# Kernel optimization log

Measured on AMD Instinct MI355X. Metric: run time of the kernel, lower is better.

Reference implementation:

```python
import jax, jax.numpy as jnp
import numpy as np

KERNEL = 3
PAD = (KERNEL - 1) // 2  # non-causal symmetric padding


def setup_inputs() -> dict:
    key = jax.random.key(0)
    k1, k2, k3 = jax.random.split(key, 3)
    B, Cin, Cout, S = 16, 64, 64, 1024
    return {
        "input": jax.random.normal(k1, (B, Cin, S), dtype=jnp.float32),
        "weight": jax.random.normal(k2, (Cout, Cin, S, KERNEL), dtype=jnp.float32),
        "bias": jax.random.normal(k3, (Cout, S), dtype=jnp.float32),
    }


def reference(input, weight, bias):
    # input: (B, Cin, S); weight: (Cout, Cin, S, K); bias: (Cout, S)
    S = input.shape[-1]
    padded = jnp.pad(input, ((0, 0), (0, 0), (PAD, PAD)))
    # unfolded windows: (B, Cin, S, K) -- small, avoids the (B,Cout,Cin,S,K) blowup
    unfolded = jnp.stack([padded[:, :, k:k + S] for k in range(KERNEL)], axis=-1)
    # position-specific (non-weight-shared) conv: contract Cin and K per position s
    out = jnp.einsum("bcsk,ocsk->bos", unfolded, weight)
    return out + bias[None, :, :]
```

## Files before the change

kernel.cpp:

```cpp
#include <hip/hip_runtime.h>

namespace {
constexpr int CIN = 64, COUT = 64, SS = 1024, KK = 3;
constexpr int STL = 16;
constexpr int CCH = 8;
constexpr int POS = STL + 2;
constexpr int RST = 20;
}

__global__ __launch_bounds__(256, 2)
void locon1d(const float* __restrict__ in, const float* __restrict__ wt,
             const float* __restrict__ bias, float* __restrict__ out) {
  __shared__ float xs[CCH * POS * RST];

  const int tid = threadIdx.x;
  const int sl  = tid & 15;
  const int og  = tid >> 4;
  const int bid = blockIdx.x;
  const int st  = bid & 63;
  const int ch  = bid >> 6;
  const int s0  = st * STL;
  const int s   = s0 + sl;
  const int cb  = ch * CCH;
  const int o0  = og * 4;

  #pragma unroll
  for (int i = 0; i < 3; ++i) {
    const int idx = tid + i * 256;
    if (idx < CCH * 4 * POS) {
      const int cg = idx / POS;
      const int p  = idx - cg * POS;
      const int g  = cg & 3;
      const int c  = cg >> 2;
      const int sg = s0 - 1 + p;
      const bool v = (unsigned)sg < (unsigned)SS;
      const float* ip = in + (size_t)(4 * g) * CIN * SS + (size_t)(cb + c) * SS + sg;
      float4 x4;
      x4.x = v ? ip[0] : 0.f;
      x4.y = v ? ip[(size_t)1 * CIN * SS] : 0.f;
      x4.z = v ? ip[(size_t)2 * CIN * SS] : 0.f;
      x4.w = v ? ip[(size_t)3 * CIN * SS] : 0.f;
      *reinterpret_cast<float4*>(&xs[(c * POS + p) * RST + 4 * g]) = x4;
    }
  }

  float w[CCH][4][KK];
  #pragma unroll
  for (int oo = 0; oo < 4; ++oo) {
    const float* wp = wt + (((size_t)(o0 + oo) * CIN + cb) * SS + s) * KK;
    #pragma unroll
    for (int c = 0; c < CCH; ++c) {
      #pragma unroll
      for (int k = 0; k < KK; ++k) w[c][oo][k] = wp[(size_t)c * SS * KK + k];
    }
  }

  float acc[4][16];
  #pragma unroll
  for (int oo = 0; oo < 4; ++oo) {
    const float bz = (ch == 0) ? bias[(o0 + oo) * SS + s] : 0.f;
    #pragma unroll
    for (int b = 0; b < 16; ++b) acc[oo][b] = bz;
  }

  __syncthreads();

  #pragma unroll
  for (int c = 0; c < CCH; ++c) {
    const float* base = &xs[(c * POS + sl) * RST];
    #pragma unroll
    for (int k = 0; k < KK; ++k) {
      #pragma unroll
      for (int g4 = 0; g4 < 4; ++g4) {
        const float4 x4 = *reinterpret_cast<const float4*>(base + k * RST + 4 * g4);
        #pragma unroll
        for (int oo = 0; oo < 4; ++oo) {
          const float wv = w[c][oo][k];
          acc[oo][4 * g4 + 0] += wv * x4.x;
          acc[oo][4 * g4 + 1] += wv * x4.y;
          acc[oo][4 * g4 + 2] += wv * x4.z;
          acc[oo][4 * g4 + 3] += wv * x4.w;
        }
      }
    }
  }

  #pragma unroll
  for (int oo = 0; oo < 4; ++oo) {
    const int o = o0 + oo;
    #pragma unroll
    for (int b = 0; b < 16; ++b) {
      atomicAdd(&out[((size_t)b * COUT + o) * SS + s], acc[oo][b]);
    }
  }
}

extern "C" void kernel_launch(void* const* d_in, const int* in_sizes, int n_in,
                              void* d_out, int out_size, void* d_ws, size_t ws_size,
                              hipStream_t stream) {
  const float* in = (const float*)d_in[0];
  const float* wt = (const float*)d_in[1];
  const float* bs = (const float*)d_in[2];
  float* out = (float*)d_out;
  hipMemsetAsync(out, 0, (size_t)out_size * sizeof(float), stream);
  hipLaunchKernelGGL(locon1d, dim3(512), dim3(256), 0, stream, in, wt, bs, out);
}
```

Baseline: 117.7 us.

## Reduce input channels in-block via shared memory instead of global atomics

Each block now covers 4 positions and all 64 input channels, split across 8 channel groups of 64 threads, and reduces their partial sums through shared memory before a single plain store per output. This removes the output memset and the 16-way global atomicAdd traffic, and bias is added at the final store. Blocks grow to 512 threads with a swizzled position mapping. The trade-off is more __syncthreads in the epilogue, only 256 blocks, and narrower per-row input loads of 6 positions.

```diff
diff --git a/kernel.cpp b/kernel.cpp
--- a/kernel.cpp
+++ b/kernel.cpp
@@ -2,95 +2,101 @@
 
 namespace {
 constexpr int CIN = 64, COUT = 64, SS = 1024, KK = 3;
-constexpr int STL = 16;
-constexpr int CCH = 8;
+constexpr int STL = 4;
 constexpr int POS = STL + 2;
-constexpr int RST = 20;
+constexpr int NCG = 8, CPG = 8;
 }
 
-__global__ __launch_bounds__(256, 2)
+__global__ __launch_bounds__(512, 2)
 void locon1d(const float* __restrict__ in, const float* __restrict__ wt,
              const float* __restrict__ bias, float* __restrict__ out) {
-  __shared__ float xs[CCH * POS * RST];
+  __shared__ float smem[8192];
 
   const int tid = threadIdx.x;
-  const int sl  = tid & 15;
-  const int og  = tid >> 4;
+  const int sl  = tid & 3;
+  const int og  = (tid >> 2) & 15;
+  const int cg  = tid >> 6;
   const int bid = blockIdx.x;
-  const int st  = bid & 63;
-  const int ch  = bid >> 6;
+  const int st  = ((bid & 7) << 5) + (bid >> 3);
   const int s0  = st * STL;
   const int s   = s0 + sl;
-  const int cb  = ch * CCH;
   const int o0  = og * 4;
+  const int cb  = cg * CPG;
 
   #pragma unroll
   for (int i = 0; i < 3; ++i) {
-    const int idx = tid + i * 256;
-    if (idx < CCH * 4 * POS) {
-      const int cg = idx / POS;
-      const int p  = idx - cg * POS;
-      const int g  = cg & 3;
-      const int c  = cg >> 2;
-      const int sg = s0 - 1 + p;
-      const bool v = (unsigned)sg < (unsigned)SS;
-      const float* ip = in + (size_t)(4 * g) * CIN * SS + (size_t)(cb + c) * SS + sg;
-      float4 x4;
-      x4.x = v ? ip[0] : 0.f;
-      x4.y = v ? ip[(size_t)1 * CIN * SS] : 0.f;
-      x4.z = v ? ip[(size_t)2 * CIN * SS] : 0.f;
-      x4.w = v ? ip[(size_t)3 * CIN * SS] : 0.f;
-      *reinterpret_cast<float4*>(&xs[(c * POS + p) * RST + 4 * g]) = x4;
-    }
+    const int t  = tid + i * 512;
+    const int c  = t / 24;
+    const int r  = t - c * 24;
+    const int bq = r / 6;
+    const int p  = r - bq * 6;
+    const int sg = s0 - 1 + p;
+    const bool v = (unsigned)sg < (unsigned)SS;
+    const float* ip = in + ((size_t)(4 * bq) * CIN + c) * SS + sg;
+    float4 x4;
+    x4.x = v ? ip[0] : 0.f;
+    x4.y = v ? ip[(size_t)1 * CIN * SS] : 0.f;
+    x4.z = v ? ip[(size_t)2 * CIN * SS] : 0.f;
+    x4.w = v ? ip[(size_t)3 * CIN * SS] : 0.f;
+    *reinterpret_cast<float4*>(&smem[(c * POS + p) * 16 + 4 * bq]) = x4;
   }
+  __syncthreads();
 
-  float w[CCH][4][KK];
+  float w[CPG][4][KK];
   #pragma unroll
   for (int oo = 0; oo < 4; ++oo) {
     const float* wp = wt + (((size_t)(o0 + oo) * CIN + cb) * SS + s) * KK;
     #pragma unroll
-    for (int c = 0; c < CCH; ++c) {
+    for (int c = 0; c < CPG; ++c)
       #pragma unroll
-      for (int k = 0; k < KK; ++k) w[c][oo][k] = wp[(size_t)c * SS * KK + k];
-    }
+      for (int k = 0; k < KK; ++k)
+        w[c][oo][k] = wp[(size_t)c * SS * KK + k];
   }
 
   float acc[4][16];
   #pragma unroll
-  for (int oo = 0; oo < 4; ++oo) {
-    const float bz = (ch == 0) ? bias[(o0 + oo) * SS + s] : 0.f;
+  for (int oo = 0; oo < 4; ++oo)
     #pragma unroll
-    for (int b = 0; b < 16; ++b) acc[oo][b] = bz;
-  }
-
-  __syncthreads();
+    for (int b = 0; b < 16; ++b) acc[oo][b] = 0.f;
 
   #pragma unroll
-  for (int c = 0; c < CCH; ++c) {
-    const float* base = &xs[(c * POS + sl) * RST];
+  for (int c = 0; c < CPG; ++c) {
     #pragma unroll
     for (int k = 0; k < KK; ++k) {
+      const float* base = &smem[((cb + c) * POS + sl + k) * 16];
       #pragma unroll
-      for (int g4 = 0; g4 < 4; ++g4) {
-        const float4 x4 = *reinterpret_cast<const float4*>(base + k * RST + 4 * g4);
+      for (int g = 0; g < 4; ++g) {
+        const float4 x4 = *reinterpret_cast<const float4*>(base + 4 * g);
         #pragma unroll
         for (int oo = 0; oo < 4; ++oo) {
           const float wv = w[c][oo][k];
-          acc[oo][4 * g4 + 0] += wv * x4.x;
-          acc[oo][4 * g4 + 1] += wv * x4.y;
-          acc[oo][4 * g4 + 2] += wv * x4.z;
-          acc[oo][4 * g4 + 3] += wv * x4.w;
+          acc[oo][4 * g + 0] += wv * x4.x;
+          acc[oo][4 * g + 1] += wv * x4.y;
+          acc[oo][4 * g + 2] += wv * x4.z;
+          acc[oo][4 * g + 3] += wv * x4.w;
         }
       }
     }
   }
 
-  #pragma unroll
+  #pragma unroll 1
   for (int oo = 0; oo < 4; ++oo) {
-    const int o = o0 + oo;
+    __syncthreads();
     #pragma unroll
-    for (int b = 0; b < 16; ++b) {
-      atomicAdd(&out[((size_t)b * COUT + o) * SS + s], acc[oo][b]);
+    for (int b = 0; b < 16; ++b)
+      smem[cg * 1024 + (b * 16 + og) * 4 + sl] = acc[oo][b];
+    __syncthreads();
+    #pragma unroll
+    for (int i = 0; i < 2; ++i) {
+      const int item = tid + i * 512;
+      float sum = 0.f;
+      #pragma unroll
+      for (int g = 0; g < NCG; ++g) sum += smem[g * 1024 + item];
+      const int b   = item >> 6;
+      const int rem = item & 63;
+      const int o   = (rem >> 2) * 4 + oo;
+      const int s2  = s0 + (rem & 3);
+      out[((size_t)b * COUT + o) * SS + s2] = sum + bias[o * SS + s2];
     }
   }
 }
@@ -102,6 +108,5 @@
   const float* wt = (const float*)d_in[1];
   const float* bs = (const float*)d_in[2];
   float* out = (float*)d_out;
-  hipMemsetAsync(out, 0, (size_t)out_size * sizeof(float), stream);
-  hipLaunchKernelGGL(locon1d, dim3(512), dim3(256), 0, stream, in, wt, bs, out);
+  hipLaunchKernelGGL(locon1d, dim3(256), dim3(512), 0, stream, in, wt, bs, out);
 }
```

Result: no change. 116.8 us (-0.8%).

## Split work by output-channel groups over full Cin, drop atomics and memset

Applied to the files above, without the earlier changes.

Each block now handles 64 positions, 4 output channels and all 64 input channels, with four batch quarters spread across waves. Weights are prefetched into registers four channels ahead and inputs are double-buffered, all read directly from global memory with no shared-memory staging. Because every block covers the full Cin reduction, outputs are written with plain stores and bias is added in the kernel, which removes the memset and the atomics. In exchange the grid drops to 256 blocks at one block per CU. Each weight is also reused across only 4 batches instead of 16, so weight traffic rises unless the caches absorb the four-fold re-reads across batch-quarter waves.

```diff
diff --git a/kernel.cpp b/kernel.cpp
--- a/kernel.cpp
+++ b/kernel.cpp
@@ -2,96 +2,86 @@
 
 namespace {
 constexpr int CIN = 64, COUT = 64, SS = 1024, KK = 3;
-constexpr int STL = 16;
-constexpr int CCH = 8;
-constexpr int POS = STL + 2;
-constexpr int RST = 20;
+constexpr int STILE = 64;
+constexpr int PF    = 4;
 }
 
-__global__ __launch_bounds__(256, 2)
+struct F3 { float x, y, z; };
+
+__global__ __launch_bounds__(256, 1)
 void locon1d(const float* __restrict__ in, const float* __restrict__ wt,
              const float* __restrict__ bias, float* __restrict__ out) {
-  __shared__ float xs[CCH * POS * RST];
+  const int tid  = threadIdx.x;
+  const int lane = tid & 63;
+  const int bq   = tid >> 6;
+  const int bid  = blockIdx.x;
+  const int st   = bid & 15;
+  const int oq   = bid >> 4;
+  const int s0   = st * STILE;
+  const int s    = s0 + lane;
+  const int o0   = oq * 4;
 
-  const int tid = threadIdx.x;
-  const int sl  = tid & 15;
-  const int og  = tid >> 4;
-  const int bid = blockIdx.x;
-  const int st  = bid & 63;
-  const int ch  = bid >> 6;
-  const int s0  = st * STL;
-  const int s   = s0 + sl;
-  const int cb  = ch * CCH;
-  const int o0  = og * 4;
+  const float* wbase = wt + (size_t)o0 * CIN * SS * KK + (size_t)s * KK;
+
+  float acc[4][4];
+  #pragma unroll
+  for (int oo = 0; oo < 4; ++oo)
+    #pragma unroll
+    for (int j = 0; j < 4; ++j) acc[oo][j] = 0.f;
+
+  F3    wv[PF][4];
+  float xv[2][4][3];
+
+  auto loadW = [&](int c, int slot) {
+    #pragma unroll
+    for (int oo = 0; oo < 4; ++oo)
+      wv[slot][oo] =
+          *reinterpret_cast<const F3*>(wbase + ((size_t)oo * CIN + c) * SS * KK);
+  };
+  auto loadX = [&](int c, int buf) {
+    #pragma unroll
+    for (int j = 0; j < 4; ++j) {
+      const float* xp = in + ((size_t)(4 * bq + j) * CIN + c) * SS;
+      #pragma unroll
+      for (int t = 0; t < 3; ++t) {
+        const int sg = s + t - 1;
+        float v = 0.f;
+        if ((unsigned)sg < (unsigned)SS) v = xp[sg];
+        xv[buf][j][t] = v;
+      }
+    }
+  };
 
   #pragma unroll
-  for (int i = 0; i < 3; ++i) {
-    const int idx = tid + i * 256;
-    if (idx < CCH * 4 * POS) {
-      const int cg = idx / POS;
-      const int p  = idx - cg * POS;
-      const int g  = cg & 3;
-      const int c  = cg >> 2;
-      const int sg = s0 - 1 + p;
-      const bool v = (unsigned)sg < (unsigned)SS;
-      const float* ip = in + (size_t)(4 * g) * CIN * SS + (size_t)(cb + c) * SS + sg;
-      float4 x4;
-      x4.x = v ? ip[0] : 0.f;
-      x4.y = v ? ip[(size_t)1 * CIN * SS] : 0.f;
-      x4.z = v ? ip[(size_t)2 * CIN * SS] : 0.f;
-      x4.w = v ? ip[(size_t)3 * CIN * SS] : 0.f;
-      *reinterpret_cast<float4*>(&xs[(c * POS + p) * RST + 4 * g]) = x4;
-    }
-  }
+  for (int c = 0; c < PF; ++c) loadW(c, c);
+  loadX(0, 0);
 
-  float w[CCH][4][KK];
-  #pragma unroll
-  for (int oo = 0; oo < 4; ++oo) {
-    const float* wp = wt + (((size_t)(o0 + oo) * CIN + cb) * SS + s) * KK;
+  for (int cc = 0; cc < CIN / PF; ++cc) {
     #pragma unroll
-    for (int c = 0; c < CCH; ++c) {
+    for (int u = 0; u < PF; ++u) {
+      const int c = cc * PF + u;
+      if (c + 1 < CIN) loadX(c + 1, (u + 1) & 1);
       #pragma unroll
-      for (int k = 0; k < KK; ++k) w[c][oo][k] = wp[(size_t)c * SS * KK + k];
-    }
-  }
-
-  float acc[4][16];
-  #pragma unroll
-  for (int oo = 0; oo < 4; ++oo) {
-    const float bz = (ch == 0) ? bias[(o0 + oo) * SS + s] : 0.f;
-    #pragma unroll
-    for (int b = 0; b < 16; ++b) acc[oo][b] = bz;
-  }
-
-  __syncthreads();
-
-  #pragma unroll
-  for (int c = 0; c < CCH; ++c) {
-    const float* base = &xs[(c * POS + sl) * RST];
-    #pragma unroll
-    for (int k = 0; k < KK; ++k) {
-      #pragma unroll
-      for (int g4 = 0; g4 < 4; ++g4) {
-        const float4 x4 = *reinterpret_cast<const float4*>(base + k * RST + 4 * g4);
+      for (int oo = 0; oo < 4; ++oo) {
+        const F3 w3 = wv[u][oo];
         #pragma unroll
-        for (int oo = 0; oo < 4; ++oo) {
-          const float wv = w[c][oo][k];
-          acc[oo][4 * g4 + 0] += wv * x4.x;
-          acc[oo][4 * g4 + 1] += wv * x4.y;
-          acc[oo][4 * g4 + 2] += wv * x4.z;
-          acc[oo][4 * g4 + 3] += wv * x4.w;
+        for (int j = 0; j < 4; ++j) {
+          acc[oo][j] += w3.x * xv[u & 1][j][0];
+          acc[oo][j] += w3.y * xv[u & 1][j][1];
+          acc[oo][j] += w3.z * xv[u & 1][j][2];
         }
       }
+      if (cc + 1 < CIN / PF) loadW(c + PF, u);
     }
   }
 
   #pragma unroll
   for (int oo = 0; oo < 4; ++oo) {
     const int o = o0 + oo;
+    const float bz = bias[(size_t)o * SS + s];
     #pragma unroll
-    for (int b = 0; b < 16; ++b) {
-      atomicAdd(&out[((size_t)b * COUT + o) * SS + s], acc[oo][b]);
-    }
+    for (int j = 0; j < 4; ++j)
+      out[((size_t)(4 * bq + j) * COUT + o) * SS + s] = acc[oo][j] + bz;
   }
 }
 
@@ -102,6 +92,5 @@
   const float* wt = (const float*)d_in[1];
   const float* bs = (const float*)d_in[2];
   float* out = (float*)d_out;
-  hipMemsetAsync(out, 0, (size_t)out_size * sizeof(float), stream);
-  hipLaunchKernelGGL(locon1d, dim3(512), dim3(256), 0, stream, in, wt, bs, out);
+  hipLaunchKernelGGL(locon1d, dim3(256), dim3(256), 0, stream, in, wt, bs, out);
 }
```

Result: no change. 118.1 us (+0.3%).
